# Kernel tuning notes

Measured on AMD Instinct MI355X. Metric: run time of the kernel, lower is better.

## Reference

```python
import jax, jax.numpy as jnp
import numpy as np

B, S, D, H = 4, 2048, 1024, 16
DK = D // H

def setup_inputs() -> dict:
    key = jax.random.key(0)
    ks = jax.random.split(key, 5)
    scale = D ** -0.5  # keep activations well-scaled for random weights
    return {
        "x": jax.random.normal(ks[0], (B, S, D), dtype=jnp.float32),
        "w_q": jax.random.normal(ks[1], (D, D), dtype=jnp.float32) * scale,
        "w_k": jax.random.normal(ks[2], (D, D), dtype=jnp.float32) * scale,
        "w_v": jax.random.normal(ks[3], (D, D), dtype=jnp.float32) * scale,
        "w_o": jax.random.normal(ks[4], (D, D), dtype=jnp.float32) * scale,
        "b_o": jnp.zeros((D,), dtype=jnp.float32),
    }

def reference(x, w_q, w_k, w_v, w_o, b_o):
    b, s, d = x.shape
    # nn.Linear applies x @ W^T; project then split heads -> [b, h, s, dk]
    q = (x @ w_q.T).reshape(b, s, H, DK).transpose(0, 2, 1, 3)
    k = (x @ w_k.T).reshape(b, s, H, DK).transpose(0, 2, 1, 3)
    v = (x @ w_v.T).reshape(b, s, H, DK).transpose(0, 2, 1, 3)
    scores = jnp.einsum('bhqd,bhkd->bhqk', q, k) * (DK ** -0.5)
    causal = jnp.tril(jnp.ones((s, s), dtype=bool))  # [s, s]
    scores = jnp.where(causal, scores, jnp.float32(-1e9))
    attn = jax.nn.softmax(scores, axis=-1)
    out = jnp.einsum('bhqk,bhkd->bhqd', attn, v)
    out = out.transpose(0, 2, 1, 3).reshape(b, s, d)
    return out @ w_o.T + b_o
```

## Files before the change

### kernel.cpp

```cpp
#include <hip/hip_runtime.h>

typedef unsigned short u16;
typedef unsigned int u32;
typedef __attribute__((ext_vector_type(4))) u16 u16x4;
typedef __attribute__((ext_vector_type(8))) short short8;
typedef __attribute__((ext_vector_type(4))) float f32x4;
typedef __attribute__((ext_vector_type(16))) float f32x16;
typedef __attribute__((ext_vector_type(4))) u32 uint4v;

#define AS1 __attribute__((address_space(1)))
#define AS3 __attribute__((address_space(3)))

#define B_  4
#define S_  2048
#define D_  1024
#define H_  16
#define DK_ 64

#define WAIT_VM(n) asm volatile("s_waitcnt vmcnt(" #n ")" ::: "memory")
#define WAIT_LGK0  asm volatile("s_waitcnt lgkmcnt(0)" ::: "memory")

__device__ __forceinline__ u16 f2bf(float f) {
  union { float f; unsigned u; } v; v.f = f;
  unsigned r = v.u + 0x7fffu + ((v.u >> 16) & 1u);
  return (u16)(r >> 16);
}

__device__ __forceinline__ u32 cvt_pk_bf16(float lo, float hi) {
  u32 r;
  asm("v_cvt_pk_bf16_f32 %0, %1, %2" : "=v"(r) : "v"(lo), "v"(hi));
  return r;
}

__device__ __forceinline__ void pl32_swap(u32& a, u32& b) {
  asm("v_permlane32_swap_b32 %0, %1" : "+v"(a), "+v"(b));
}

__device__ __forceinline__ void gload_lds16(const void* g, void* l) {
  __builtin_amdgcn_global_load_lds((const AS1 void*)g, (AS3 void*)l, 16, 0, 0);
}

__global__ __launch_bounds__(256) void conv_bf16(const float* __restrict__ in,
                                                 u16* __restrict__ out,
                                                 int n, float scale) {
  int i = (blockIdx.x * 256 + threadIdx.x) * 8;
  if (i >= n) return;
  f32x4 a = *reinterpret_cast<const f32x4*>(in + i);
  f32x4 b = *reinterpret_cast<const f32x4*>(in + i + 4);
  union { u16 u[8]; uint4v v; } r;
#pragma unroll
  for (int j = 0; j < 4; ++j) {
    r.u[j]     = f2bf(a[j] * scale);
    r.u[4 + j] = f2bf(b[j] * scale);
  }
  *reinterpret_cast<uint4v*>(out + i) = r.v;
}

__global__ __launch_bounds__(256) void conv_w4(const float* __restrict__ w0,
                                               const float* __restrict__ w1,
                                               const float* __restrict__ w2,
                                               const float* __restrict__ w3,
                                               u16* __restrict__ out, float s0) {
  int y = blockIdx.y;
  const float* src = (y == 0) ? w0 : (y == 1) ? w1 : (y == 2) ? w2 : w3;
  float scale = (y == 0) ? s0 : 1.0f;
  int i = (blockIdx.x * 256 + threadIdx.x) * 8;
  f32x4 a = *reinterpret_cast<const f32x4*>(src + i);
  f32x4 b = *reinterpret_cast<const f32x4*>(src + i + 4);
  union { u16 u[8]; uint4v v; } r;
#pragma unroll
  for (int j = 0; j < 4; ++j) {
    r.u[j]     = f2bf(a[j] * scale);
    r.u[4 + j] = f2bf(b[j] * scale);
  }
  *reinterpret_cast<uint4v*>(out + (size_t)y * (D_ * D_) + i) = r.v;
}

__global__ __launch_bounds__(512, 2) void gemm_qkv(const u16* __restrict__ A,
                                                   const u16* __restrict__ B,
                                                   u16* __restrict__ Qb,
                                                   u16* __restrict__ Kb,
                                                   u16* __restrict__ Vt,
                                                   int M, int N, int K, int nbx) {
  __shared__ __attribute__((aligned(16))) u16 As[2][256 * 64];
  __shared__ __attribute__((aligned(16))) u16 Bs[2][256 * 64];

  const int t = threadIdx.x;
  const int l = t & 63;
  const int w = t >> 6;
  const int wm = w >> 2;
  const int wn = w & 3;
  const int dd = blockIdx.x;
  const int cpx = gridDim.x >> 3;
  const int lid = (dd & 7) * cpx + (dd >> 3);
  const int m0 = (lid / nbx) * 256;
  const int n0 = (lid % nbx) * 256;
  const int NT = K >> 6;

  f32x4 zero = {0.f, 0.f, 0.f, 0.f};
  f32x4 acc[8][4];
#pragma unroll
  for (int i = 0; i < 8; ++i)
#pragma unroll
    for (int j = 0; j < 4; ++j) acc[i][j] = zero;

  auto stage = [&](int kt, int buf) {
#pragma unroll
    for (int i = 0; i < 4; ++i) {
      int slot = i * 512 + t;
      int r = slot >> 3, c = slot & 7;
      gload_lds16(A + (size_t)(m0 + r) * K + kt * 64 + ((c ^ (r & 7)) * 8),
                  (char*)&As[buf][0] + (size_t)(i * 512 + w * 64) * 16);
      gload_lds16(B + (size_t)(n0 + r) * K + kt * 64 + ((c ^ (r & 7)) * 8),
                  (char*)&Bs[buf][0] + (size_t)(i * 512 + w * 64) * 16);
    }
  };

  stage(0, 0);

  for (int kt = 0; kt < NT; ++kt) {
    const int buf = kt & 1;
    WAIT_VM(0);
    __builtin_amdgcn_s_barrier();
    __builtin_amdgcn_sched_barrier(0);
    if (kt + 1 < NT) stage(kt + 1, buf ^ 1);

#pragma unroll
    for (int kc = 0; kc < 2; ++kc) {
      short8 a[8], bfr[4];
      int lc = kc * 4 + (l >> 4);
#pragma unroll
      for (int i = 0; i < 8; ++i) {
        int ra = wm * 128 + i * 16 + (l & 15);
        a[i] = *reinterpret_cast<const short8*>(&As[buf][ra * 64 + ((lc ^ (ra & 7)) * 8)]);
      }
#pragma unroll
      for (int i = 0; i < 4; ++i) {
        int rb = wn * 64 + i * 16 + (l & 15);
        bfr[i] = *reinterpret_cast<const short8*>(&Bs[buf][rb * 64 + ((lc ^ (rb & 7)) * 8)]);
      }
#pragma unroll
      for (int mi = 0; mi < 8; ++mi)
#pragma unroll
        for (int ni = 0; ni < 4; ++ni)
          acc[mi][ni] = __builtin_amdgcn_mfma_f32_16x16x32_bf16(a[mi], bfr[ni], acc[mi][ni], 0, 0, 0);
    }
  }

#pragma unroll
  for (int ni = 0; ni < 4; ++ni) {
    int col = n0 + wn * 64 + ni * 16 + (l & 15);
#pragma unroll
    for (int mi = 0; mi < 8; ++mi) {
      int row0 = m0 + wm * 128 + mi * 16 + (l >> 4) * 4;
      if (col < 2048) {
        u16* dst = (col < 1024) ? Qb : Kb;
        int c = col & 1023;
#pragma unroll
        for (int r = 0; r < 4; ++r)
          dst[(size_t)(row0 + r) * 1024 + c] = f2bf(acc[mi][ni][r]);
      } else {
        int vc = col - 2048;
        int bh = (row0 >> 11) * 16 + (vc >> 6);
        int s0 = row0 & 2047;
        u16x4 pk;
#pragma unroll
        for (int r = 0; r < 4; ++r) pk[r] = f2bf(acc[mi][ni][r]);
        *reinterpret_cast<u16x4*>(Vt + ((size_t)(bh * 64 + (vc & 63))) * 2048 + s0) = pk;
      }
    }
  }
}

__global__ __launch_bounds__(256) void gemm_op(const u16* __restrict__ A,
                                               const u16* __restrict__ B,
                                               float* __restrict__ Cf,
                                               const float* __restrict__ bias,
                                               int M, int N, int K, int nbx) {
  __shared__ __attribute__((aligned(16))) u16 As[2][128 * 64];
  __shared__ __attribute__((aligned(16))) u16 Bs[2][128 * 64];

  const int t = threadIdx.x;
  const int l = t & 63;
  const int w = t >> 6;
  const int wr = w >> 1, wc = w & 1;
  const int dd = blockIdx.x;
  const int cpx = gridDim.x >> 3;
  const int lid = (dd & 7) * cpx + (dd >> 3);
  const int m0 = (lid / nbx) * 128;
  const int n0 = (lid % nbx) * 128;
  const int NT = K >> 6;

  f32x4 zero = {0.f, 0.f, 0.f, 0.f};
  f32x4 acc[4][4];
#pragma unroll
  for (int i = 0; i < 4; ++i)
#pragma unroll
    for (int j = 0; j < 4; ++j) acc[i][j] = zero;

  auto stage = [&](int kt, int buf) {
#pragma unroll
    for (int i = 0; i < 4; ++i) {
      int slot = i * 256 + t;
      int r = slot >> 3, c = slot & 7;
      gload_lds16(A + (size_t)(m0 + r) * K + kt * 64 + ((c ^ (r & 7)) * 8),
                  (char*)&As[buf][0] + (size_t)(i * 256 + w * 64) * 16);
      gload_lds16(B + (size_t)(n0 + r) * K + kt * 64 + ((c ^ (r & 7)) * 8),
                  (char*)&Bs[buf][0] + (size_t)(i * 256 + w * 64) * 16);
    }
  };

  stage(0, 0);
  stage(1, 1);

  for (int kt = 0; kt < NT; ++kt) {
    const int buf = kt & 1;
    if (kt < NT - 1) { WAIT_VM(8); } else { WAIT_VM(0); }
    __builtin_amdgcn_s_barrier();
    __builtin_amdgcn_sched_barrier(0);

#pragma unroll
    for (int kc = 0; kc < 2; ++kc) {
      short8 a[4], bf[4];
      int lc = kc * 4 + (l >> 4);
#pragma unroll
      for (int i = 0; i < 4; ++i) {
        int ra = wr * 64 + i * 16 + (l & 15);
        a[i] = *reinterpret_cast<const short8*>(&As[buf][ra * 64 + ((lc ^ (ra & 7)) * 8)]);
        int rb = wc * 64 + i * 16 + (l & 15);
        bf[i] = *reinterpret_cast<const short8*>(&Bs[buf][rb * 64 + ((lc ^ (rb & 7)) * 8)]);
      }
#pragma unroll
      for (int mi = 0; mi < 4; ++mi)
#pragma unroll
        for (int ni = 0; ni < 4; ++ni)
          acc[mi][ni] = __builtin_amdgcn_mfma_f32_16x16x32_bf16(a[mi], bf[ni], acc[mi][ni], 0, 0, 0);
    }

    WAIT_LGK0;
    __builtin_amdgcn_sched_barrier(0);
    __builtin_amdgcn_s_barrier();
    if (kt + 2 < NT) stage(kt + 2, buf);
  }

#pragma unroll
  for (int ni = 0; ni < 4; ++ni) {
    int col = n0 + wc * 64 + ni * 16 + (l & 15);
    float bv = bias[col];
#pragma unroll
    for (int mi = 0; mi < 4; ++mi) {
      int row0 = m0 + wr * 64 + mi * 16 + (l >> 4) * 4;
#pragma unroll
      for (int r = 0; r < 4; ++r)
        Cf[(size_t)(row0 + r) * N + col] = acc[mi][ni][r] + bv;
    }
  }
}

__global__ __launch_bounds__(512) void attn_fwd(const u16* __restrict__ Q,
                                                const u16* __restrict__ K,
                                                const u16* __restrict__ Vtg,
                                                u16* __restrict__ AO) {
  __shared__ __attribute__((aligned(16))) u16 smem[24576];
  u16* Ksb = smem;
  u16* Vsb = smem + 12288;

  const int t = threadIdx.x;
  const int l = t & 63;
  const int w = t >> 6;
  const int hi = l >> 5;
  const int hi8 = hi * 8, hi4 = hi * 4;
  const int bh = blockIdx.x;
  const int by = blockIdx.y;
  const int s = (by < 4) ? (7 - 2 * by) : (2 * (by - 4));
  const size_t qkbase = (size_t)((bh >> 4) * S_) * D_ + (bh & 15) * DK_;
  const u16* Vg = Vtg + (size_t)bh * 64 * S_;

  const int qw = s * 256 + w * 32;
  const int qi = qw + (l & 31);

  short8 qf[4];
#pragma unroll
  for (int c = 0; c < 4; ++c)
    qf[c] = *reinterpret_cast<const short8*>(Q + qkbase + (size_t)qi * D_ + c * 16 + hi8);

  f32x16 o0 = {0,0,0,0,0,0,0,0,0,0,0,0,0,0,0,0};
  f32x16 o1 = {0,0,0,0,0,0,0,0,0,0,0,0,0,0,0,0};
  float l_r = 0.f;

  const int nst = 4 * (s + 1);

  auto stage = [&](int jt, u16* kdst, u16* vdst) {
    const u16* Ksrc = K + qkbase + (size_t)(jt * 64) * D_;
    const u16* Vsrc = Vg + jt * 64;
    int r = t >> 3, c = t & 7;
    gload_lds16(Ksrc + (size_t)r * D_ + ((c ^ (r & 7)) * 8),
                (char*)kdst + (size_t)t * 16);
    gload_lds16(Vsrc + (size_t)r * S_ + ((c ^ (r & 7)) * 8),
                (char*)vdst + (size_t)t * 16);
  };

  stage(0, Ksb, Vsb);
  stage(1, Ksb + 4096, Vsb + 4096);
  stage(2, Ksb + 8192, Vsb + 8192);
  int o0b = 0, o1b = 4096, o2b = 8192;

  for (int it = 0; it < nst; ++it) {
    if (it < nst - 2)       { WAIT_VM(4); }
    else if (it == nst - 2) { WAIT_VM(2); }
    else                    { WAIT_VM(0); }
    __builtin_amdgcn_s_barrier();
    __builtin_amdgcn_sched_barrier(0);

    const int j0 = it * 64;
    u16* ks = Ksb + o0b;
    u16* vs = Vsb + o0b;

    if (j0 <= qw + 31) {
      f32x16 s0 = {0,0,0,0,0,0,0,0,0,0,0,0,0,0,0,0};
      f32x16 s1 = {0,0,0,0,0,0,0,0,0,0,0,0,0,0,0,0};
#pragma unroll
      for (int c = 0; c < 4; ++c) {
        int cl = 2 * c + hi;
        int k0r = l & 31, k1r = (l & 31) + 32;
        short8 kf0 = *reinterpret_cast<const short8*>(&ks[k0r * 64 + ((cl ^ (k0r & 7)) * 8)]);
        short8 kf1 = *reinterpret_cast<const short8*>(&ks[k1r * 64 + ((cl ^ (k1r & 7)) * 8)]);
        s0 = __builtin_amdgcn_mfma_f32_32x32x16_bf16(kf0, qf[c], s0, 0, 0, 0);
        s1 = __builtin_amdgcn_mfma_f32_32x32x16_bf16(kf1, qf[c], s1, 0, 0, 0);
      }
      if (j0 + 63 > qw) {
#pragma unroll
        for (int r = 0; r < 16; ++r) {
          int key = j0 + (r & 3) + 8 * (r >> 2) + hi4;
          if (key > qi) s0[r] = -INFINITY;
          if (key + 32 > qi) s1[r] = -INFINITY;
        }
      }
      {
        float sum = 0.f;
#pragma unroll
        for (int r = 0; r < 16; ++r) { s0[r] = exp2f(s0[r]); sum += s0[r]; }
#pragma unroll
        for (int r = 0; r < 16; ++r) { s1[r] = exp2f(s1[r]); sum += s1[r]; }
        sum += __shfl_xor(sum, 32);
        l_r += sum;
      }
#pragma unroll
      for (int ksl = 0; ksl < 4; ++ksl) {
        const int b = 8 * (ksl & 1);
        const f32x16& ps = (ksl < 2) ? s0 : s1;
        u32 c0 = cvt_pk_bf16(ps[b + 0], ps[b + 1]);
        u32 c1 = cvt_pk_bf16(ps[b + 2], ps[b + 3]);
        u32 c2 = cvt_pk_bf16(ps[b + 4], ps[b + 5]);
        u32 c3 = cvt_pk_bf16(ps[b + 6], ps[b + 7]);
        pl32_swap(c0, c2);
        pl32_swap(c1, c3);
        union { u32 u[4]; short8 s; } pa;
        pa.u[0] = c0; pa.u[1] = c1; pa.u[2] = c2; pa.u[3] = c3;
        int cl = 2 * ksl + hi;
        int d0r = l & 31, d1r = (l & 31) + 32;
        short8 vf0 = *reinterpret_cast<const short8*>(&vs[d0r * 64 + ((cl ^ (d0r & 7)) * 8)]);
        short8 vf1 = *reinterpret_cast<const short8*>(&vs[d1r * 64 + ((cl ^ (d1r & 7)) * 8)]);
        o0 = __builtin_amdgcn_mfma_f32_32x32x16_bf16(vf0, pa.s, o0, 0, 0, 0);
        o1 = __builtin_amdgcn_mfma_f32_32x32x16_bf16(vf1, pa.s, o1, 0, 0, 0);
      }
    }

    WAIT_LGK0;
    __builtin_amdgcn_sched_barrier(0);
    __builtin_amdgcn_s_barrier();
    if (it + 3 < nst) stage(it + 3, Ksb + o0b, Vsb + o0b);
    int tmp = o0b; o0b = o1b; o1b = o2b; o2b = tmp;
  }

  float inv = 1.0f / l_r;
  u16* Ob = smem + w * 2304;
#pragma unroll
  for (int acc = 0; acc < 2; ++acc) {
    const f32x16& oo = acc ? o1 : o0;
#pragma unroll
    for (int rp = 0; rp < 8; ++rp) {
      u32 pk = cvt_pk_bf16(oo[2 * rp] * inv, oo[2 * rp + 1] * inv);
      int d0 = ((2 * rp) & 3) + 8 * (rp >> 1) + hi4 + 32 * acc;
      *reinterpret_cast<u32*>(&Ob[(l & 31) * 72 + d0]) = pk;
    }
  }
  __syncthreads();
  int qq = l >> 1;
  int chb = (l & 1) * 4;
#pragma unroll
  for (int c2 = 0; c2 < 4; ++c2) {
    uint4v vv = *reinterpret_cast<const uint4v*>(&Ob[qq * 72 + (chb + c2) * 8]);
    *reinterpret_cast<uint4v*>(&AO[qkbase + (size_t)(qw + qq) * D_ + (chb + c2) * 8]) = vv;
  }
}

extern "C" void kernel_launch(void* const* d_in, const int* in_sizes, int n_in,
                              void* d_out, int out_size, void* d_ws, size_t ws_size,
                              hipStream_t stream) {
  const float* x  = (const float*)d_in[0];
  const float* wq = (const float*)d_in[1];
  const float* wk = (const float*)d_in[2];
  const float* wv = (const float*)d_in[3];
  const float* wo = (const float*)d_in[4];
  const float* bo = (const float*)d_in[5];
  float* out = (float*)d_out;

  char* ws = (char*)d_ws;
  u16* XB   = (u16*)(ws);
  u16* WQKV = (u16*)(ws + (size_t)(16 << 20));
  u16* WOB  = (u16*)(ws + (size_t)(22 << 20));
  u16* Qb   = (u16*)(ws + (size_t)(24 << 20));
  u16* Kb   = (u16*)(ws + (size_t)(40 << 20));
  u16* Vt   = (u16*)(ws + (size_t)(56 << 20));
  u16* AO   = (u16*)(ws + (size_t)(72 << 20));

  const int nx = B_ * S_ * D_;
  const int nw = D_ * D_;

  conv_bf16<<<nx / 2048, 256, 0, stream>>>(x, XB, nx, 1.0f);
  conv_w4<<<dim3(nw / 2048, 4), 256, 0, stream>>>(wq, wk, wv, wo, WQKV,
                                                  0.18033688011112042f);

  gemm_qkv<<<384, 512, 0, stream>>>(
      XB, WQKV, Qb, Kb, Vt, B_ * S_, 3072, D_, 12);

  attn_fwd<<<dim3(B_ * H_, 8), 512, 0, stream>>>(Qb, Kb, Vt, AO);

  gemm_op<<<512, 256, 0, stream>>>(
      AO, WOB, out, bo, B_ * S_, D_, D_, 8);
}
```

Measured before the change: 177.0 us.

## Split QKV GEMM tiles into half-tile quadrants with staggered prefetch pipeline

Splits the A and B LDS tiles of the QKV projection GEMM into 128-row halves. Each k-step now runs as four quadrant phases, and each phase issues the next iteration's global-to-LDS load for one half-tile. Fine-grained vmcnt waits, barriers and s_setprio around the MFMA blocks let loads overlap compute. The warp-to-output mapping changes to match, and the epilogue indexing is updated. This adds barriers per k-step and more complex wait-count bookkeeping.

```diff
diff --git a/kernel.cpp b/kernel.cpp
--- a/kernel.cpp
+++ b/kernel.cpp
@@ -82,8 +82,8 @@
                                                    u16* __restrict__ Kb,
                                                    u16* __restrict__ Vt,
                                                    int M, int N, int K, int nbx) {
-  __shared__ __attribute__((aligned(16))) u16 As[2][256 * 64];
-  __shared__ __attribute__((aligned(16))) u16 Bs[2][256 * 64];
+  __shared__ __attribute__((aligned(16))) u16 As[2][2][128 * 64];
+  __shared__ __attribute__((aligned(16))) u16 Bs[2][2][128 * 64];
 
   const int t = threadIdx.x;
   const int l = t & 63;
@@ -104,55 +104,83 @@
 #pragma unroll
     for (int j = 0; j < 4; ++j) acc[i][j] = zero;
 
-  auto stage = [&](int kt, int buf) {
-#pragma unroll
-    for (int i = 0; i < 4; ++i) {
+  auto stageH = [&](int kt, int sidx, int d) {
+    const bool isA = ((sidx & 1) == 0);
+    const int h = sidx >> 1;
+    const u16* src = isA ? (A + (size_t)(m0 + h * 128) * K)
+                         : (B + (size_t)(n0 + h * 128) * K);
+    u16* dst = isA ? &As[d][h][0] : &Bs[d][h][0];
+#pragma unroll
+    for (int i = 0; i < 2; ++i) {
       int slot = i * 512 + t;
       int r = slot >> 3, c = slot & 7;
-      gload_lds16(A + (size_t)(m0 + r) * K + kt * 64 + ((c ^ (r & 7)) * 8),
-                  (char*)&As[buf][0] + (size_t)(i * 512 + w * 64) * 16);
-      gload_lds16(B + (size_t)(n0 + r) * K + kt * 64 + ((c ^ (r & 7)) * 8),
-                  (char*)&Bs[buf][0] + (size_t)(i * 512 + w * 64) * 16);
+      gload_lds16(src + (size_t)r * K + kt * 64 + ((c ^ (r & 7)) * 8),
+                  (char*)dst + (size_t)(i * 512 + w * 64) * 16);
     }
   };
 
-  stage(0, 0);
+  stageH(0, 0, 0);
+  stageH(0, 1, 0);
+  stageH(0, 2, 0);
+  stageH(0, 3, 0);
+  WAIT_VM(4);
+  __builtin_amdgcn_s_barrier();
 
   for (int kt = 0; kt < NT; ++kt) {
     const int buf = kt & 1;
-    WAIT_VM(0);
-    __builtin_amdgcn_s_barrier();
-    __builtin_amdgcn_sched_barrier(0);
-    if (kt + 1 < NT) stage(kt + 1, buf ^ 1);
-
-#pragma unroll
-    for (int kc = 0; kc < 2; ++kc) {
-      short8 a[8], bfr[4];
-      int lc = kc * 4 + (l >> 4);
-#pragma unroll
-      for (int i = 0; i < 8; ++i) {
-        int ra = wm * 128 + i * 16 + (l & 15);
-        a[i] = *reinterpret_cast<const short8*>(&As[buf][ra * 64 + ((lc ^ (ra & 7)) * 8)]);
-      }
-#pragma unroll
-      for (int i = 0; i < 4; ++i) {
-        int rb = wn * 64 + i * 16 + (l & 15);
-        bfr[i] = *reinterpret_cast<const short8*>(&Bs[buf][rb * 64 + ((lc ^ (rb & 7)) * 8)]);
-      }
-#pragma unroll
-      for (int mi = 0; mi < 8; ++mi)
-#pragma unroll
-        for (int ni = 0; ni < 4; ++ni)
-          acc[mi][ni] = __builtin_amdgcn_mfma_f32_16x16x32_bf16(a[mi], bfr[ni], acc[mi][ni], 0, 0, 0);
+    const bool pf = (kt + 1 < NT);
+#pragma unroll
+    for (int q = 0; q < 4; ++q) {
+      const int a = (q == 1 || q == 2) ? 1 : 0;
+      const int b = (q >= 2) ? 1 : 0;
+
+      short8 af[4][2], bfr[2][2];
+#pragma unroll
+      for (int kc = 0; kc < 2; ++kc) {
+        int lc = kc * 4 + (l >> 4);
+#pragma unroll
+        for (int mi = 0; mi < 4; ++mi) {
+          int ra = wm * 64 + mi * 16 + (l & 15);
+          af[mi][kc] = *reinterpret_cast<const short8*>(
+              &As[buf][a][ra * 64 + ((lc ^ (ra & 7)) * 8)]);
+        }
+#pragma unroll
+        for (int ni = 0; ni < 2; ++ni) {
+          int rb = wn * 32 + ni * 16 + (l & 15);
+          bfr[ni][kc] = *reinterpret_cast<const short8*>(
+              &Bs[buf][b][rb * 64 + ((lc ^ (rb & 7)) * 8)]);
+        }
+      }
+      if (pf) stageH(kt + 1, q, buf ^ 1);
+
+      __builtin_amdgcn_s_barrier();
+      WAIT_LGK0;
+      __builtin_amdgcn_sched_barrier(0);
+      __builtin_amdgcn_s_setprio(1);
+#pragma unroll
+      for (int kc = 0; kc < 2; ++kc)
+#pragma unroll
+        for (int mi = 0; mi < 4; ++mi)
+#pragma unroll
+          for (int ni = 0; ni < 2; ++ni)
+            acc[a * 4 + mi][b * 2 + ni] = __builtin_amdgcn_mfma_f32_16x16x32_bf16(
+                af[mi][kc], bfr[ni][kc], acc[a * 4 + mi][b * 2 + ni], 0, 0, 0);
+      __builtin_amdgcn_s_setprio(0);
+
+      if (q == 0)      { if (pf) { WAIT_VM(4); } else { WAIT_VM(2); } }
+      else if (q == 1) { if (pf) { WAIT_VM(4); } else { WAIT_VM(0); } }
+      else if (q == 3) { if (pf) { WAIT_VM(4); } }
+      __builtin_amdgcn_sched_barrier(0);
+      __builtin_amdgcn_s_barrier();
     }
   }
 
 #pragma unroll
   for (int ni = 0; ni < 4; ++ni) {
-    int col = n0 + wn * 64 + ni * 16 + (l & 15);
+    int col = n0 + (ni >> 1) * 128 + wn * 32 + (ni & 1) * 16 + (l & 15);
 #pragma unroll
     for (int mi = 0; mi < 8; ++mi) {
-      int row0 = m0 + wm * 128 + mi * 16 + (l >> 4) * 4;
+      int row0 = m0 + (mi >> 2) * 128 + wm * 64 + (mi & 3) * 16 + (l >> 4) * 4;
       if (col < 2048) {
         u16* dst = (col < 1024) ? Qb : Kb;
         int c = col & 1023;
```

After: 177.2 us. Within noise of the previous version (+0.1%).
